# Kernel tuning notes

Measured on AMD Instinct MI355X. Metric: run time of the kernel, lower is better.

Reference implementation:

```python
import jax, jax.numpy as jnp
import numpy as np

N_NODES = 100000
N_EDGES = 1600000
N_GRAPHS = 512
IN_DIM = 128
HID = 128
N_CLASSES = 10


def _gcn_conv(x, W, b, src, dst, n):
    """PyG GCNConv: out = D^{-1/2} (A+I) D^{-1/2} (x @ W) + b."""
    xw = x @ W  # [n, out_dim]
    loop = jnp.arange(n)
    s = jnp.concatenate([src, loop])  # add self loops
    d = jnp.concatenate([dst, loop])
    deg = jax.ops.segment_sum(jnp.ones(s.shape, dtype=xw.dtype), d, num_segments=n)
    dinv = jnp.where(deg > 0, jax.lax.rsqrt(deg), jnp.zeros((), xw.dtype))
    norm = dinv[s] * dinv[d]  # [E + n]
    out = jax.ops.segment_sum(xw[s] * norm[:, None], d, num_segments=n)
    return out + b


def _global_mean_pool(x, batch, num_graphs):
    sums = jax.ops.segment_sum(x, batch, num_segments=num_graphs)
    cnts = jax.ops.segment_sum(jnp.ones(batch.shape, dtype=x.dtype), batch, num_segments=num_graphs)
    return sums / jnp.maximum(cnts, 1.0)[:, None]


def setup_inputs() -> dict:
    key = jax.random.key(0)
    ks = jax.random.split(key, 8)
    x = jax.random.normal(ks[0], (N_NODES, IN_DIM), dtype=jnp.float32)
    edge_index = jax.random.randint(ks[1], (2, N_EDGES), 0, N_NODES, dtype=jnp.int64)
    batch = jnp.sort(jax.random.randint(ks[2], (N_NODES,), 0, N_GRAPHS, dtype=jnp.int64))
    sc = 1.0 / np.sqrt(IN_DIM)
    W1 = jax.random.normal(ks[3], (IN_DIM, HID), dtype=jnp.float32) * sc
    b1 = jnp.zeros((HID,), dtype=jnp.float32)
    W2 = jax.random.normal(ks[4], (HID, HID), dtype=jnp.float32) * (1.0 / np.sqrt(HID))
    b2 = jnp.zeros((HID,), dtype=jnp.float32)
    Wc = jax.random.normal(ks[5], (HID, N_CLASSES), dtype=jnp.float32) * (1.0 / np.sqrt(HID))
    bc = jnp.zeros((N_CLASSES,), dtype=jnp.float32)
    return {"x": x, "edge_index": edge_index, "batch": batch,
            "W1": W1, "b1": b1, "W2": W2, "b2": b2, "Wc": Wc, "bc": bc}


def reference(x, edge_index, batch, W1, b1, W2, b2, Wc, bc):
    src, dst = edge_index[0], edge_index[1]
    n = x.shape[0]
    h = _gcn_conv(x, W1, b1, src, dst, n)
    h = jax.nn.relu(h)
    h = _gcn_conv(h, W2, b2, src, dst, n)
    g = _global_mean_pool(h, batch, N_GRAPHS)
    return g @ Wc + bc
```

## Files before the change

kernel.cpp:

```cpp
#include <hip/hip_runtime.h>

#define N_NODES 100000
#define N_EDGES 1600000
#define N_GRAPHS 512
#define DIM 128
#define NCLS 10
#define NBKT 782
#define BCAP 2560

typedef __attribute__((ext_vector_type(8))) short short8;
typedef __attribute__((ext_vector_type(4))) float f32x4;

static __device__ __forceinline__ unsigned short f2bf(float f) {
    unsigned u = __float_as_uint(f);
    unsigned r = (u + 0x7FFF + ((u >> 16) & 1)) >> 16;
    return (unsigned short)r;
}
static __device__ __forceinline__ float bf2f(unsigned u) {
    return __uint_as_float(u << 16);
}


__global__ void k_wprep(const float* __restrict__ W1, const float* __restrict__ W2,
                        unsigned short* __restrict__ wf1, unsigned short* __restrict__ wf2,
                        int* __restrict__ bcnt) {
    int b = blockIdx.x;
    if (b >= 128) {
        int i = (b - 128) * 256 + threadIdx.x;
        if (i < NBKT) bcnt[i] = 0;
        return;
    }
    const float* W = (b < 64) ? W1 : W2;
    unsigned short* wfrag = (b < 64) ? wf1 : wf2;
    int t = (b & 63) * 256 + threadIdx.x;
    int j = t & 7, lane = (t >> 3) & 63, nt = (t >> 9) & 7, kit = t >> 12;
    int k = kit * 32 + (lane >> 4) * 8 + j;
    int n = nt * 16 + (lane & 15);
    float v = W[k * 128 + n];
    unsigned short h = f2bf(v);
    wfrag[t] = h;
    wfrag[16384 + t] = f2bf(v - bf2f(h));
}


__global__ __launch_bounds__(256) void k_bucket(
    const int* __restrict__ src, const int* __restrict__ dst,
    int* __restrict__ bcnt, unsigned* __restrict__ bpack, int E) {
    __shared__ int cnt[NBKT];
    __shared__ int base[NBKT];
    int tid = threadIdx.x;
    for (int i = tid; i < NBKT; i += 256) cnt[i] = 0;
    __syncthreads();
    int e0 = blockIdx.x * 4096 + tid;
    unsigned pk[16]; short bk[16];
#pragma unroll
    for (int j = 0; j < 16; j++) {
        int e = e0 + j * 256;
        if (e < E) {
            int s = src[e], d = dst[e];
            bk[j] = (short)(d >> 7);
            pk[j] = ((unsigned)(d & 127) << 17) | (unsigned)s;
            atomicAdd(&cnt[bk[j]], 1);
        } else bk[j] = -1;
    }
    __syncthreads();
    for (int i = tid; i < NBKT; i += 256) {
        int c = cnt[i];
        base[i] = c ? atomicAdd(&bcnt[i], c) : 0;
        cnt[i] = 0;
    }
    __syncthreads();
#pragma unroll
    for (int j = 0; j < 16; j++) {
        if (bk[j] >= 0) {
            int p = base[bk[j]] + atomicAdd(&cnt[bk[j]], 1);
            if (p < BCAP) bpack[(size_t)bk[j] * BCAP + p] = pk[j];
        }
    }
}


__global__ __launch_bounds__(256) void k_bsort(
    const unsigned* __restrict__ bpack, const int* __restrict__ bcnt,
    int* __restrict__ rp, float* __restrict__ dinv,
    int* __restrict__ esrc, int N) {
    __shared__ int lds[256];
    __shared__ int gbase_sh;
    __shared__ int cnt[128];
    __shared__ int scan[128];
    __shared__ int cur[128];
    int b = blockIdx.x, tid = threadIdx.x;
    int v[4], pre[4];
    int s = 0;
#pragma unroll
    for (int j = 0; j < 4; j++) {
        int idx = tid * 4 + j;
        v[j] = (idx < NBKT) ? min(bcnt[idx], BCAP) : 0;
        pre[j] = s; s += v[j];
    }
    lds[tid] = s;
    __syncthreads();
    for (int off = 1; off < 256; off <<= 1) {
        int t = (tid >= off) ? lds[tid - off] : 0;
        __syncthreads();
        lds[tid] += t;
        __syncthreads();
    }
    if (tid == (b >> 2)) gbase_sh = lds[tid] - s + pre[b & 3];
    if (tid < 128) cnt[tid] = 0;
    __syncthreads();
    int gbase = gbase_sh;
    int n0 = b << 7;
    int m = min(bcnt[b], BCAP);
    const unsigned* bp = bpack + (size_t)b * BCAP;
    for (int j = tid; j < m; j += 256) atomicAdd(&cnt[bp[j] >> 17], 1);
    __syncthreads();
    if (tid < 128) scan[tid] = cnt[tid];
    __syncthreads();
    for (int off = 1; off < 128; off <<= 1) {
        int t = (tid < 128 && tid >= off) ? scan[tid - off] : 0;
        __syncthreads();
        if (tid < 128) scan[tid] += t;
        __syncthreads();
    }
    if (tid < 128) {
        int c = cnt[tid];
        int excl = scan[tid] - c;
        int node = n0 + tid;
        if (node <= N) rp[node] = gbase + excl;
        if (node < N) dinv[node] = rsqrtf((float)(c + 1));
        cur[tid] = gbase + excl;
    }
    __syncthreads();
    for (int j = tid; j < m; j += 256) {
        unsigned pk = bp[j];
        int p = atomicAdd(&cur[pk >> 17], 1);
        esrc[p] = (int)(pk & 0x1FFFF);
    }
}


__global__ __launch_bounds__(256) void k_gemm_f32(
    const float* __restrict__ A, const unsigned short* __restrict__ wfrag,
    const float* __restrict__ dinv, unsigned short* __restrict__ ybf, int M) {
    __shared__ unsigned short ldsw[4 * 32 * 136];
    int tid = threadIdx.x, wave = tid >> 6, lane = tid & 63;
    int m = lane & 15, quad = lane >> 4;
    int rowBase = blockIdx.x * 128 + wave * 32;
    int r0 = rowBase + m, r1 = rowBase + 16 + m;
    for (int i = tid; i < 2048; i += 256)
        ((short8*)ldsw)[i] = ((const short8*)wfrag)[i];
    __syncthreads();
    f32x4 acc0[8], acc1[8];
#pragma unroll
    for (int i = 0; i < 8; i++) { acc0[i] = (f32x4){0,0,0,0}; acc1[i] = (f32x4){0,0,0,0}; }
    const unsigned short* wlo = wfrag + 16384;

#pragma unroll
    for (int kit = 0; kit < 4; kit++) {
        float a0[8], a1[8];
        if (r0 < M) {
            const float4* ap = (const float4*)(A + (size_t)r0 * 128 + kit * 32 + quad * 8);
            float4 f0 = ap[0], f1 = ap[1];
            a0[0]=f0.x; a0[1]=f0.y; a0[2]=f0.z; a0[3]=f0.w; a0[4]=f1.x; a0[5]=f1.y; a0[6]=f1.z; a0[7]=f1.w;
        } else { for (int j = 0; j < 8; j++) a0[j] = 0.f; }
        if (r1 < M) {
            const float4* ap = (const float4*)(A + (size_t)r1 * 128 + kit * 32 + quad * 8);
            float4 f0 = ap[0], f1 = ap[1];
            a1[0]=f0.x; a1[1]=f0.y; a1[2]=f0.z; a1[3]=f0.w; a1[4]=f1.x; a1[5]=f1.y; a1[6]=f1.z; a1[7]=f1.w;
        } else { for (int j = 0; j < 8; j++) a1[j] = 0.f; }
        short8 ahi0, alo0, ahi1, alo1;
#pragma unroll
        for (int j = 0; j < 8; j++) {
            unsigned short h0 = f2bf(a0[j]);
            ahi0[j] = (short)h0; alo0[j] = (short)f2bf(a0[j] - bf2f(h0));
            unsigned short h1 = f2bf(a1[j]);
            ahi1[j] = (short)h1; alo1[j] = (short)f2bf(a1[j] - bf2f(h1));
        }
        int fb = kit * 4096 + lane * 8;
#pragma unroll
        for (int nt = 0; nt < 8; nt++) {
            int idx = fb + nt * 512;
            short8 bhi = *(const short8*)(ldsw + idx);
            short8 blo = *(const short8*)(wlo + idx);
            acc0[nt] = __builtin_amdgcn_mfma_f32_16x16x32_bf16(ahi0, bhi, acc0[nt], 0, 0, 0);
            acc0[nt] = __builtin_amdgcn_mfma_f32_16x16x32_bf16(alo0, bhi, acc0[nt], 0, 0, 0);
            acc0[nt] = __builtin_amdgcn_mfma_f32_16x16x32_bf16(ahi0, blo, acc0[nt], 0, 0, 0);
            acc1[nt] = __builtin_amdgcn_mfma_f32_16x16x32_bf16(ahi1, bhi, acc1[nt], 0, 0, 0);
            acc1[nt] = __builtin_amdgcn_mfma_f32_16x16x32_bf16(alo1, bhi, acc1[nt], 0, 0, 0);
            acc1[nt] = __builtin_amdgcn_mfma_f32_16x16x32_bf16(ahi1, blo, acc1[nt], 0, 0, 0);
        }
    }
    __syncthreads();
    float dv0 = (r0 < M) ? dinv[r0] : 0.f;
    float dv1 = (r1 < M) ? dinv[r1] : 0.f;
    unsigned short* wsm = ldsw + wave * 32 * 136;
#pragma unroll
    for (int rg = 0; rg < 4; rg++) {
        float s0 = __shfl(dv0, quad * 4 + rg);
        float s1 = __shfl(dv1, quad * 4 + rg);
#pragma unroll
        for (int nt = 0; nt < 8; nt++) {
            wsm[(quad * 4 + rg) * 136 + nt * 16 + m] = f2bf(acc0[nt][rg] * s0);
            wsm[(16 + quad * 4 + rg) * 136 + nt * 16 + m] = f2bf(acc1[nt][rg] * s1);
        }
    }
    __syncthreads();
#pragma unroll
    for (int i = 0; i < 8; i++) {
        int rl = i * 4 + quad;
        int grow = rowBase + rl;
        if (grow < M) {
            short8 v = *(const short8*)(wsm + rl * 136 + m * 8);
            *(short8*)(ybf + (size_t)grow * 128 + m * 8) = v;
        }
    }
}


__global__ __launch_bounds__(256) void k_gemm_bf(
    const unsigned short* __restrict__ A, const unsigned short* __restrict__ wfrag,
    const float* __restrict__ dinv, unsigned short* __restrict__ ybf, int M) {
    __shared__ unsigned short ldsw[4 * 32 * 136];
    int tid = threadIdx.x, wave = tid >> 6, lane = tid & 63;
    int m = lane & 15, quad = lane >> 4;
    int rowBase = blockIdx.x * 128 + wave * 32;
    int r0 = rowBase + m, r1 = rowBase + 16 + m;
    for (int i = tid; i < 2048; i += 256)
        ((short8*)ldsw)[i] = ((const short8*)wfrag)[i];
    __syncthreads();
    f32x4 acc0[8], acc1[8];
#pragma unroll
    for (int i = 0; i < 8; i++) { acc0[i] = (f32x4){0,0,0,0}; acc1[i] = (f32x4){0,0,0,0}; }
    const unsigned short* wlo = wfrag + 16384;

#pragma unroll
    for (int kit = 0; kit < 4; kit++) {
        short8 ah0, ah1;
        if (r0 < M) ah0 = *(const short8*)(A + (size_t)r0 * 128 + kit * 32 + quad * 8);
        else { for (int j = 0; j < 8; j++) ah0[j] = 0; }
        if (r1 < M) ah1 = *(const short8*)(A + (size_t)r1 * 128 + kit * 32 + quad * 8);
        else { for (int j = 0; j < 8; j++) ah1[j] = 0; }
        int fb = kit * 4096 + lane * 8;
#pragma unroll
        for (int nt = 0; nt < 8; nt++) {
            int idx = fb + nt * 512;
            short8 bhi = *(const short8*)(ldsw + idx);
            short8 blo = *(const short8*)(wlo + idx);
            acc0[nt] = __builtin_amdgcn_mfma_f32_16x16x32_bf16(ah0, bhi, acc0[nt], 0, 0, 0);
            acc0[nt] = __builtin_amdgcn_mfma_f32_16x16x32_bf16(ah0, blo, acc0[nt], 0, 0, 0);
            acc1[nt] = __builtin_amdgcn_mfma_f32_16x16x32_bf16(ah1, bhi, acc1[nt], 0, 0, 0);
            acc1[nt] = __builtin_amdgcn_mfma_f32_16x16x32_bf16(ah1, blo, acc1[nt], 0, 0, 0);
        }
    }
    __syncthreads();
    float dv0 = (r0 < M) ? dinv[r0] : 0.f;
    float dv1 = (r1 < M) ? dinv[r1] : 0.f;
    unsigned short* wsm = ldsw + wave * 32 * 136;
#pragma unroll
    for (int rg = 0; rg < 4; rg++) {
        float s0 = __shfl(dv0, quad * 4 + rg);
        float s1 = __shfl(dv1, quad * 4 + rg);
#pragma unroll
        for (int nt = 0; nt < 8; nt++) {
            wsm[(quad * 4 + rg) * 136 + nt * 16 + m] = f2bf(acc0[nt][rg] * s0);
            wsm[(16 + quad * 4 + rg) * 136 + nt * 16 + m] = f2bf(acc1[nt][rg] * s1);
        }
    }
    __syncthreads();
#pragma unroll
    for (int i = 0; i < 8; i++) {
        int rl = i * 4 + quad;
        int grow = rowBase + rl;
        if (grow < M) {
            short8 v = *(const short8*)(wsm + rl * 136 + m * 8);
            *(short8*)(ybf + (size_t)grow * 128 + m * 8) = v;
        }
    }
}


__global__ __launch_bounds__(256) void k_agg(
    const unsigned short* __restrict__ y, const float* __restrict__ dinv,
    const int* __restrict__ rp, const int* __restrict__ esrc,
    const float* __restrict__ bias, unsigned* __restrict__ out, int relu, int N) {
    int wave = threadIdx.x >> 6;
    int lane = threadIdx.x & 63;
    int node = blockIdx.x * 4 + wave;
    if (node >= N) return;
    const unsigned* y2 = (const unsigned*)y;
    unsigned vs = y2[(size_t)node * 64 + lane];
    float a0 = bf2f(vs & 0xFFFF), a1 = bf2f(vs >> 16);
    int beg = rp[node], end = rp[node + 1];
    int j = beg;
    while (j < end) {
        int idxv = (j + lane < end) ? esrc[j + lane] : 0;
        int cnt = end - j; if (cnt > 64) cnt = 64;
        int i = 0;
        for (; i + 4 <= cnt; i += 4) {
            int s0 = __shfl(idxv, i + 0);
            int s1 = __shfl(idxv, i + 1);
            int s2 = __shfl(idxv, i + 2);
            int s3 = __shfl(idxv, i + 3);
            unsigned v0 = y2[(size_t)s0 * 64 + lane];
            unsigned v1 = y2[(size_t)s1 * 64 + lane];
            unsigned v2 = y2[(size_t)s2 * 64 + lane];
            unsigned v3 = y2[(size_t)s3 * 64 + lane];
            a0 += bf2f(v0 & 0xFFFF); a1 += bf2f(v0 >> 16);
            a0 += bf2f(v1 & 0xFFFF); a1 += bf2f(v1 >> 16);
            a0 += bf2f(v2 & 0xFFFF); a1 += bf2f(v2 >> 16);
            a0 += bf2f(v3 & 0xFFFF); a1 += bf2f(v3 >> 16);
        }
        for (; i < cnt; i++) {
            int s = __shfl(idxv, i);
            unsigned v = y2[(size_t)s * 64 + lane];
            a0 += bf2f(v & 0xFFFF); a1 += bf2f(v >> 16);
        }
        j += cnt;
    }
    float s = dinv[node];
    float2 bv = ((const float2*)bias)[lane];
    float o0 = s * a0 + bv.x;
    float o1 = s * a1 + bv.y;
    if (relu) { o0 = fmaxf(o0, 0.f); o1 = fmaxf(o1, 0.f); }
    out[(size_t)node * 64 + lane] = (unsigned)f2bf(o0) | ((unsigned)f2bf(o1) << 16);
}


__global__ __launch_bounds__(256) void k_poolhead(
    const unsigned* __restrict__ h2, const int* __restrict__ batch,
    const float* __restrict__ Wc, const float* __restrict__ bc,
    float* __restrict__ out, int n) {
    __shared__ float2 red[4][64];
    __shared__ float grow[DIM];
    int gid = blockIdx.x;
    int tid = threadIdx.x, wave = tid >> 6, lane = tid & 63;
    int lo = 0, hi = n;
    while (lo < hi) { int mid = (lo + hi) >> 1; if (batch[mid] < gid) lo = mid + 1; else hi = mid; }
    int start = lo;
    hi = n;
    while (lo < hi) { int mid = (lo + hi) >> 1; if (batch[mid] < gid + 1) lo = mid + 1; else hi = mid; }
    int end = lo;
    float a0 = 0.f, a1 = 0.f;
    for (int r = start + wave; r < end; r += 4) {
        unsigned v = h2[(size_t)r * 64 + lane];
        a0 += bf2f(v & 0xFFFF); a1 += bf2f(v >> 16);
    }
    red[wave][lane] = make_float2(a0, a1);
    __syncthreads();
    if (tid < 64) {
        float2 s = red[0][tid];
        s.x += red[1][tid].x; s.y += red[1][tid].y;
        s.x += red[2][tid].x; s.y += red[2][tid].y;
        s.x += red[3][tid].x; s.y += red[3][tid].y;
        int cnt = end - start;
        float inv = 1.f / (float)(cnt > 0 ? cnt : 1);
        grow[tid * 2] = s.x * inv;
        grow[tid * 2 + 1] = s.y * inv;
    }
    __syncthreads();
    if (tid < NCLS) {
        float acc = bc[tid];
#pragma unroll 16
        for (int k = 0; k < DIM; k++) acc += grow[k] * Wc[k * NCLS + tid];
        out[gid * NCLS + tid] = acc;
    }
}

extern "C" void kernel_launch(void* const* d_in, const int* in_sizes, int n_in,
                              void* d_out, int out_size, void* d_ws, size_t ws_size,
                              hipStream_t stream) {
    const float* x    = (const float*)d_in[0];
    const int*   ei   = (const int*)d_in[1];
    const int*   batch= (const int*)d_in[2];
    const float* W1   = (const float*)d_in[3];
    const float* b1   = (const float*)d_in[4];
    const float* W2   = (const float*)d_in[5];
    const float* b2   = (const float*)d_in[6];
    const float* Wc   = (const float*)d_in[7];
    const float* bc   = (const float*)d_in[8];
    float* out = (float*)d_out;
    const int N = N_NODES, E = N_EDGES;
    const int* src = ei;
    const int* dst = ei + E;

    char* ws = (char*)d_ws;
    size_t off = 0;
    auto carve = [&](size_t bytes) -> void* {
        void* p = ws + off;
        off = (off + bytes + 255) & ~(size_t)255;
        return p;
    };
    int*      rp    = (int*)     carve((size_t)(N + 1) * 4);
    float*    dinv  = (float*)   carve((size_t)N * 4);
    int*      bcnt  = (int*)     carve(NBKT * 4);
    unsigned* bpack = (unsigned*)carve((size_t)NBKT * BCAP * 4);
    int*      esrc  = (int*)     carve((size_t)E * 4);
    unsigned short* wf1 = (unsigned short*)carve(2 * 16384 * 2);
    unsigned short* wf2 = (unsigned short*)carve(2 * 16384 * 2);
    unsigned short* bufY = (unsigned short*)carve((size_t)N * DIM * 2);
    unsigned short* bufH = (unsigned short*)carve((size_t)N * DIM * 2);
    (void)ws_size; (void)n_in; (void)in_sizes; (void)out_size;

    hipLaunchKernelGGL(k_wprep,  dim3(128 + (NBKT + 255) / 256), dim3(256), 0, stream, W1, W2, wf1, wf2, bcnt);
    hipLaunchKernelGGL(k_bucket, dim3((E + 4095) / 4096), dim3(256), 0, stream, src, dst, bcnt, bpack, E);
    hipLaunchKernelGGL(k_bsort,  dim3(NBKT), dim3(256), 0, stream, bpack, bcnt, rp, dinv, esrc, N);

    int gemmGrid = (N + 127) / 128;
    hipLaunchKernelGGL(k_gemm_f32, dim3(gemmGrid), dim3(256), 0, stream, x, wf1, dinv, bufY, N);
    hipLaunchKernelGGL(k_agg, dim3((N + 3) / 4), dim3(256), 0, stream, bufY, dinv, rp, esrc, b1, (unsigned*)bufH, 1, N);
    hipLaunchKernelGGL(k_gemm_bf, dim3(gemmGrid), dim3(256), 0, stream, bufH, wf2, dinv, bufY, N);
    hipLaunchKernelGGL(k_agg, dim3((N + 3) / 4), dim3(256), 0, stream, bufY, dinv, rp, esrc, b2, (unsigned*)bufH, 0, N);
    hipLaunchKernelGGL(k_poolhead, dim3(N_GRAPHS), dim3(256), 0, stream, (const unsigned*)bufH, batch, Wc, bc, out, N);
}
```

Baseline: 340.9 us.

## Overlap first GEMM with graph bucketing/sort by merging kernels; move dinv scaling into aggregation

The source-side dinv scaling is moved out of both GEMM epilogues and into the aggregation kernels, which now gather dinv[src] per edge and scale each neighbour row. This removes the GEMMs' dependence on dinv. The first GEMM is then split in half and fused as extra blocks into the bucket and bucket-sort launches, so its work overlaps the CSR construction and saves a kernel launch. The cost is an extra dinv gather per edge and more multiplies in the gather loop of both aggregation passes.

Result: no change. 344.2 us (+1.0%).

```diff
diff --git a/kernel.cpp b/kernel.cpp
--- a/kernel.cpp
+++ b/kernel.cpp
@@ -43,15 +43,16 @@
 }
 
 
-__global__ __launch_bounds__(256) void k_bucket(
+static __device__ __forceinline__ void bucket_body(
+    char* smemraw, int bid,
     const int* __restrict__ src, const int* __restrict__ dst,
     int* __restrict__ bcnt, unsigned* __restrict__ bpack, int E) {
-    __shared__ int cnt[NBKT];
-    __shared__ int base[NBKT];
+    int* cnt  = (int*)smemraw;
+    int* base = cnt + NBKT;
     int tid = threadIdx.x;
     for (int i = tid; i < NBKT; i += 256) cnt[i] = 0;
     __syncthreads();
-    int e0 = blockIdx.x * 4096 + tid;
+    int e0 = bid * 4096 + tid;
     unsigned pk[16]; short bk[16];
 #pragma unroll
     for (int j = 0; j < 16; j++) {
@@ -79,17 +80,17 @@
     }
 }
 
-
-__global__ __launch_bounds__(256) void k_bsort(
+static __device__ __forceinline__ void bsort_body(
+    char* smemraw, int b,
     const unsigned* __restrict__ bpack, const int* __restrict__ bcnt,
     int* __restrict__ rp, float* __restrict__ dinv,
     int* __restrict__ esrc, int N) {
-    __shared__ int lds[256];
-    __shared__ int gbase_sh;
-    __shared__ int cnt[128];
-    __shared__ int scan[128];
-    __shared__ int cur[128];
-    int b = blockIdx.x, tid = threadIdx.x;
+    int* lds      = (int*)smemraw;
+    int* cnt      = lds + 256;
+    int* scan     = lds + 384;
+    int* cur      = lds + 512;
+    int* gbase_sh = lds + 640;
+    int tid = threadIdx.x;
     int v[4], pre[4];
     int s = 0;
 #pragma unroll
@@ -106,10 +107,10 @@
         lds[tid] += t;
         __syncthreads();
     }
-    if (tid == (b >> 2)) gbase_sh = lds[tid] - s + pre[b & 3];
+    if (tid == (b >> 2)) *gbase_sh = lds[tid] - s + pre[b & 3];
     if (tid < 128) cnt[tid] = 0;
     __syncthreads();
-    int gbase = gbase_sh;
+    int gbase = *gbase_sh;
     int n0 = b << 7;
     int m = min(bcnt[b], BCAP);
     const unsigned* bp = bpack + (size_t)b * BCAP;
@@ -139,14 +140,14 @@
     }
 }
 
-
-__global__ __launch_bounds__(256) void k_gemm_f32(
+static __device__ __forceinline__ void gemm_f32_body(
+    char* smemraw, int rowBlk,
     const float* __restrict__ A, const unsigned short* __restrict__ wfrag,
-    const float* __restrict__ dinv, unsigned short* __restrict__ ybf, int M) {
-    __shared__ unsigned short ldsw[4 * 32 * 136];
+    unsigned short* __restrict__ ybf, int M) {
+    unsigned short* ldsw = (unsigned short*)smemraw;
     int tid = threadIdx.x, wave = tid >> 6, lane = tid & 63;
     int m = lane & 15, quad = lane >> 4;
-    int rowBase = blockIdx.x * 128 + wave * 32;
+    int rowBase = rowBlk * 128 + wave * 32;
     int r0 = rowBase + m, r1 = rowBase + 16 + m;
     for (int i = tid; i < 2048; i += 256)
         ((short8*)ldsw)[i] = ((const short8*)wfrag)[i];
@@ -192,17 +193,13 @@
         }
     }
     __syncthreads();
-    float dv0 = (r0 < M) ? dinv[r0] : 0.f;
-    float dv1 = (r1 < M) ? dinv[r1] : 0.f;
     unsigned short* wsm = ldsw + wave * 32 * 136;
 #pragma unroll
     for (int rg = 0; rg < 4; rg++) {
-        float s0 = __shfl(dv0, quad * 4 + rg);
-        float s1 = __shfl(dv1, quad * 4 + rg);
 #pragma unroll
         for (int nt = 0; nt < 8; nt++) {
-            wsm[(quad * 4 + rg) * 136 + nt * 16 + m] = f2bf(acc0[nt][rg] * s0);
-            wsm[(16 + quad * 4 + rg) * 136 + nt * 16 + m] = f2bf(acc1[nt][rg] * s1);
+            wsm[(quad * 4 + rg) * 136 + nt * 16 + m] = f2bf(acc0[nt][rg]);
+            wsm[(16 + quad * 4 + rg) * 136 + nt * 16 + m] = f2bf(acc1[nt][rg]);
         }
     }
     __syncthreads();
@@ -218,9 +215,31 @@
 }
 
 
+__global__ __launch_bounds__(256) void k_p2(
+    const int* __restrict__ src, const int* __restrict__ dst,
+    int* __restrict__ bcnt, unsigned* __restrict__ bpack, int E,
+    const float* __restrict__ A, const unsigned short* __restrict__ wfrag,
+    unsigned short* __restrict__ ybf, int M, int nb) {
+    __shared__ __align__(16) char smem[4 * 32 * 136 * 2];
+    if ((int)blockIdx.x < nb) bucket_body(smem, blockIdx.x, src, dst, bcnt, bpack, E);
+    else                      gemm_f32_body(smem, blockIdx.x - nb, A, wfrag, ybf, M);
+}
+
+
+__global__ __launch_bounds__(256) void k_p3(
+    const unsigned* __restrict__ bpack, const int* __restrict__ bcnt,
+    int* __restrict__ rp, float* __restrict__ dinv, int* __restrict__ esrc, int N,
+    const float* __restrict__ A, const unsigned short* __restrict__ wfrag,
+    unsigned short* __restrict__ ybf, int M, int rowOff) {
+    __shared__ __align__(16) char smem[4 * 32 * 136 * 2];
+    if ((int)blockIdx.x < NBKT) bsort_body(smem, blockIdx.x, bpack, bcnt, rp, dinv, esrc, N);
+    else                        gemm_f32_body(smem, rowOff + (blockIdx.x - NBKT), A, wfrag, ybf, M);
+}
+
+
 __global__ __launch_bounds__(256) void k_gemm_bf(
     const unsigned short* __restrict__ A, const unsigned short* __restrict__ wfrag,
-    const float* __restrict__ dinv, unsigned short* __restrict__ ybf, int M) {
+    unsigned short* __restrict__ ybf, int M) {
     __shared__ unsigned short ldsw[4 * 32 * 136];
     int tid = threadIdx.x, wave = tid >> 6, lane = tid & 63;
     int m = lane & 15, quad = lane >> 4;
@@ -254,17 +273,13 @@
         }
     }
     __syncthreads();
-    float dv0 = (r0 < M) ? dinv[r0] : 0.f;
-    float dv1 = (r1 < M) ? dinv[r1] : 0.f;
     unsigned short* wsm = ldsw + wave * 32 * 136;
 #pragma unroll
     for (int rg = 0; rg < 4; rg++) {
-        float s0 = __shfl(dv0, quad * 4 + rg);
-        float s1 = __shfl(dv1, quad * 4 + rg);
 #pragma unroll
         for (int nt = 0; nt < 8; nt++) {
-            wsm[(quad * 4 + rg) * 136 + nt * 16 + m] = f2bf(acc0[nt][rg] * s0);
-            wsm[(16 + quad * 4 + rg) * 136 + nt * 16 + m] = f2bf(acc1[nt][rg] * s1);
+            wsm[(quad * 4 + rg) * 136 + nt * 16 + m] = f2bf(acc0[nt][rg]);
+            wsm[(16 + quad * 4 + rg) * 136 + nt * 16 + m] = f2bf(acc1[nt][rg]);
         }
     }
     __syncthreads();
@@ -289,12 +304,14 @@
     int node = blockIdx.x * 4 + wave;
     if (node >= N) return;
     const unsigned* y2 = (const unsigned*)y;
+    float sd = dinv[node];
     unsigned vs = y2[(size_t)node * 64 + lane];
-    float a0 = bf2f(vs & 0xFFFF), a1 = bf2f(vs >> 16);
+    float a0 = sd * bf2f(vs & 0xFFFF), a1 = sd * bf2f(vs >> 16);
     int beg = rp[node], end = rp[node + 1];
     int j = beg;
     while (j < end) {
-        int idxv = (j + lane < end) ? esrc[j + lane] : 0;
+        int idxv = 0; float dvv = 0.f;
+        if (j + lane < end) { idxv = esrc[j + lane]; dvv = dinv[idxv]; }
         int cnt = end - j; if (cnt > 64) cnt = 64;
         int i = 0;
         for (; i + 4 <= cnt; i += 4) {
@@ -302,26 +319,30 @@
             int s1 = __shfl(idxv, i + 1);
             int s2 = __shfl(idxv, i + 2);
             int s3 = __shfl(idxv, i + 3);
+            float d0 = __shfl(dvv, i + 0);
+            float d1 = __shfl(dvv, i + 1);
+            float d2 = __shfl(dvv, i + 2);
+            float d3 = __shfl(dvv, i + 3);
             unsigned v0 = y2[(size_t)s0 * 64 + lane];
             unsigned v1 = y2[(size_t)s1 * 64 + lane];
             unsigned v2 = y2[(size_t)s2 * 64 + lane];
             unsigned v3 = y2[(size_t)s3 * 64 + lane];
-            a0 += bf2f(v0 & 0xFFFF); a1 += bf2f(v0 >> 16);
-            a0 += bf2f(v1 & 0xFFFF); a1 += bf2f(v1 >> 16);
-            a0 += bf2f(v2 & 0xFFFF); a1 += bf2f(v2 >> 16);
-            a0 += bf2f(v3 & 0xFFFF); a1 += bf2f(v3 >> 16);
+            a0 += d0 * bf2f(v0 & 0xFFFF); a1 += d0 * bf2f(v0 >> 16);
+            a0 += d1 * bf2f(v1 & 0xFFFF); a1 += d1 * bf2f(v1 >> 16);
+            a0 += d2 * bf2f(v2 & 0xFFFF); a1 += d2 * bf2f(v2 >> 16);
+            a0 += d3 * bf2f(v3 & 0xFFFF); a1 += d3 * bf2f(v3 >> 16);
         }
         for (; i < cnt; i++) {
             int s = __shfl(idxv, i);
+            float d = __shfl(dvv, i);
             unsigned v = y2[(size_t)s * 64 + lane];
-            a0 += bf2f(v & 0xFFFF); a1 += bf2f(v >> 16);
+            a0 += d * bf2f(v & 0xFFFF); a1 += d * bf2f(v >> 16);
         }
         j += cnt;
     }
-    float s = dinv[node];
     float2 bv = ((const float2*)bias)[lane];
-    float o0 = s * a0 + bv.x;
-    float o1 = s * a1 + bv.y;
+    float o0 = sd * a0 + bv.x;
+    float o1 = sd * a1 + bv.y;
     if (relu) { o0 = fmaxf(o0, 0.f); o1 = fmaxf(o1, 0.f); }
     out[(size_t)node * 64 + lane] = (unsigned)f2bf(o0) | ((unsigned)f2bf(o1) << 16);
 }
@@ -402,14 +423,17 @@
     unsigned short* bufH = (unsigned short*)carve((size_t)N * DIM * 2);
     (void)ws_size; (void)n_in; (void)in_sizes; (void)out_size;
 
-    hipLaunchKernelGGL(k_wprep,  dim3(128 + (NBKT + 255) / 256), dim3(256), 0, stream, W1, W2, wf1, wf2, bcnt);
-    hipLaunchKernelGGL(k_bucket, dim3((E + 4095) / 4096), dim3(256), 0, stream, src, dst, bcnt, bpack, E);
-    hipLaunchKernelGGL(k_bsort,  dim3(NBKT), dim3(256), 0, stream, bpack, bcnt, rp, dinv, esrc, N);
-
-    int gemmGrid = (N + 127) / 128;
-    hipLaunchKernelGGL(k_gemm_f32, dim3(gemmGrid), dim3(256), 0, stream, x, wf1, dinv, bufY, N);
+    const int nbBkt = (E + 4095) / 4096;
+    const int gemmGrid = (N + 127) / 128;
+    const int gA = gemmGrid / 2;
+
+    hipLaunchKernelGGL(k_wprep, dim3(128 + (NBKT + 255) / 256), dim3(256), 0, stream, W1, W2, wf1, wf2, bcnt);
+    hipLaunchKernelGGL(k_p2, dim3(nbBkt + gA), dim3(256), 0, stream,
+                       src, dst, bcnt, bpack, E, x, wf1, bufY, N, nbBkt);
+    hipLaunchKernelGGL(k_p3, dim3(NBKT + (gemmGrid - gA)), dim3(256), 0, stream,
+                       bpack, bcnt, rp, dinv, esrc, N, x, wf1, bufY, N, gA);
     hipLaunchKernelGGL(k_agg, dim3((N + 3) / 4), dim3(256), 0, stream, bufY, dinv, rp, esrc, b1, (unsigned*)bufH, 1, N);
-    hipLaunchKernelGGL(k_gemm_bf, dim3(gemmGrid), dim3(256), 0, stream, bufH, wf2, dinv, bufY, N);
+    hipLaunchKernelGGL(k_gemm_bf, dim3(gemmGrid), dim3(256), 0, stream, bufH, wf2, bufY, N);
     hipLaunchKernelGGL(k_agg, dim3((N + 3) / 4), dim3(256), 0, stream, bufY, dinv, rp, esrc, b2, (unsigned*)bufH, 0, N);
     hipLaunchKernelGGL(k_poolhead, dim3(N_GRAPHS), dim3(256), 0, stream, (const unsigned*)bufH, batch, Wc, bc, out, N);
 }
```

## Merge bucket sort and first GEMM into one launch using global degree counts

Applied to the files above, without the earlier changes.

The first GEMM needs only node degrees, so degrees are now counted with global atomics during bucketing. This lets the bucket-sort blocks and the layer-1 GEMM blocks run side by side in one heterogeneous kernel instead of two dependent launches. The goal is to overlap the latency-bound sort with the compute-bound GEMM and save one launch. The cost is 1.6M extra global atomics on the degree array, one more zeroing pass, and a shared LDS size across both block types.

Result: slower. 386.4 us (+13.4%).

```diff
diff --git a/kernel.cpp b/kernel.cpp
--- a/kernel.cpp
+++ b/kernel.cpp
@@ -23,11 +23,16 @@
 
 __global__ void k_wprep(const float* __restrict__ W1, const float* __restrict__ W2,
                         unsigned short* __restrict__ wf1, unsigned short* __restrict__ wf2,
-                        int* __restrict__ bcnt) {
+                        int* __restrict__ bcnt, int* __restrict__ deg) {
     int b = blockIdx.x;
     if (b >= 128) {
-        int i = (b - 128) * 256 + threadIdx.x;
-        if (i < NBKT) bcnt[i] = 0;
+        if (b < 132) {
+            int i = (b - 128) * 256 + threadIdx.x;
+            if (i < NBKT) bcnt[i] = 0;
+        } else {
+            int i = (b - 132) * 256 + threadIdx.x;
+            if (i < N_NODES) deg[i] = 0;
+        }
         return;
     }
     const float* W = (b < 64) ? W1 : W2;
@@ -45,7 +50,8 @@
 
 __global__ __launch_bounds__(256) void k_bucket(
     const int* __restrict__ src, const int* __restrict__ dst,
-    int* __restrict__ bcnt, unsigned* __restrict__ bpack, int E) {
+    int* __restrict__ bcnt, unsigned* __restrict__ bpack,
+    int* __restrict__ deg, int E) {
     __shared__ int cnt[NBKT];
     __shared__ int base[NBKT];
     int tid = threadIdx.x;
@@ -58,6 +64,7 @@
         int e = e0 + j * 256;
         if (e < E) {
             int s = src[e], d = dst[e];
+            atomicAdd(&deg[d], 1);
             bk[j] = (short)(d >> 7);
             pk[j] = ((unsigned)(d & 127) << 17) | (unsigned)s;
             atomicAdd(&cnt[bk[j]], 1);
@@ -80,16 +87,17 @@
 }
 
 
-__global__ __launch_bounds__(256) void k_bsort(
+static __device__ __forceinline__ void bsort_body(
+    char* smemraw, int b,
     const unsigned* __restrict__ bpack, const int* __restrict__ bcnt,
     int* __restrict__ rp, float* __restrict__ dinv,
     int* __restrict__ esrc, int N) {
-    __shared__ int lds[256];
-    __shared__ int gbase_sh;
-    __shared__ int cnt[128];
-    __shared__ int scan[128];
-    __shared__ int cur[128];
-    int b = blockIdx.x, tid = threadIdx.x;
+    int* lds      = (int*)smemraw;
+    int* cnt      = lds + 256;
+    int* scan     = lds + 384;
+    int* cur      = lds + 512;
+    int* gbase_sh = lds + 640;
+    int tid = threadIdx.x;
     int v[4], pre[4];
     int s = 0;
 #pragma unroll
@@ -106,10 +114,10 @@
         lds[tid] += t;
         __syncthreads();
     }
-    if (tid == (b >> 2)) gbase_sh = lds[tid] - s + pre[b & 3];
+    if (tid == (b >> 2)) *gbase_sh = lds[tid] - s + pre[b & 3];
     if (tid < 128) cnt[tid] = 0;
     __syncthreads();
-    int gbase = gbase_sh;
+    int gbase = *gbase_sh;
     int n0 = b << 7;
     int m = min(bcnt[b], BCAP);
     const unsigned* bp = bpack + (size_t)b * BCAP;
@@ -139,14 +147,14 @@
     }
 }
 
-
-__global__ __launch_bounds__(256) void k_gemm_f32(
+static __device__ __forceinline__ void gemm_f32_body(
+    char* smemraw, int rowBlk,
     const float* __restrict__ A, const unsigned short* __restrict__ wfrag,
-    const float* __restrict__ dinv, unsigned short* __restrict__ ybf, int M) {
-    __shared__ unsigned short ldsw[4 * 32 * 136];
+    const int* __restrict__ deg, unsigned short* __restrict__ ybf, int M) {
+    unsigned short* ldsw = (unsigned short*)smemraw;
     int tid = threadIdx.x, wave = tid >> 6, lane = tid & 63;
     int m = lane & 15, quad = lane >> 4;
-    int rowBase = blockIdx.x * 128 + wave * 32;
+    int rowBase = rowBlk * 128 + wave * 32;
     int r0 = rowBase + m, r1 = rowBase + 16 + m;
     for (int i = tid; i < 2048; i += 256)
         ((short8*)ldsw)[i] = ((const short8*)wfrag)[i];
@@ -192,8 +200,8 @@
         }
     }
     __syncthreads();
-    float dv0 = (r0 < M) ? dinv[r0] : 0.f;
-    float dv1 = (r1 < M) ? dinv[r1] : 0.f;
+    float dv0 = (r0 < M) ? rsqrtf((float)deg[r0] + 1.0f) : 0.f;
+    float dv1 = (r1 < M) ? rsqrtf((float)deg[r1] + 1.0f) : 0.f;
     unsigned short* wsm = ldsw + wave * 32 * 136;
 #pragma unroll
     for (int rg = 0; rg < 4; rg++) {
@@ -215,6 +223,17 @@
             *(short8*)(ybf + (size_t)grow * 128 + m * 8) = v;
         }
     }
+}
+
+
+__global__ __launch_bounds__(256) void k_p3(
+    const unsigned* __restrict__ bpack, const int* __restrict__ bcnt,
+    int* __restrict__ rp, float* __restrict__ dinv, int* __restrict__ esrc, int N,
+    const float* __restrict__ A, const unsigned short* __restrict__ wfrag,
+    const int* __restrict__ deg, unsigned short* __restrict__ ybf, int M) {
+    __shared__ __align__(16) char smem[4 * 32 * 136 * 2];
+    if ((int)blockIdx.x < NBKT) bsort_body(smem, blockIdx.x, bpack, bcnt, rp, dinv, esrc, N);
+    else                        gemm_f32_body(smem, blockIdx.x - NBKT, A, wfrag, deg, ybf, M);
 }
 
 
@@ -394,6 +413,7 @@
     int*      rp    = (int*)     carve((size_t)(N + 1) * 4);
     float*    dinv  = (float*)   carve((size_t)N * 4);
     int*      bcnt  = (int*)     carve(NBKT * 4);
+    int*      deg   = (int*)     carve((size_t)N * 4);
     unsigned* bpack = (unsigned*)carve((size_t)NBKT * BCAP * 4);
     int*      esrc  = (int*)     carve((size_t)E * 4);
     unsigned short* wf1 = (unsigned short*)carve(2 * 16384 * 2);
@@ -402,12 +422,14 @@
     unsigned short* bufH = (unsigned short*)carve((size_t)N * DIM * 2);
     (void)ws_size; (void)n_in; (void)in_sizes; (void)out_size;
 
-    hipLaunchKernelGGL(k_wprep,  dim3(128 + (NBKT + 255) / 256), dim3(256), 0, stream, W1, W2, wf1, wf2, bcnt);
-    hipLaunchKernelGGL(k_bucket, dim3((E + 4095) / 4096), dim3(256), 0, stream, src, dst, bcnt, bpack, E);
-    hipLaunchKernelGGL(k_bsort,  dim3(NBKT), dim3(256), 0, stream, bpack, bcnt, rp, dinv, esrc, N);
-
-    int gemmGrid = (N + 127) / 128;
-    hipLaunchKernelGGL(k_gemm_f32, dim3(gemmGrid), dim3(256), 0, stream, x, wf1, dinv, bufY, N);
+    const int nbBkt = (E + 4095) / 4096;
+    const int gemmGrid = (N + 127) / 128;
+    const int degZero = (N + 255) / 256;
+
+    hipLaunchKernelGGL(k_wprep, dim3(132 + degZero), dim3(256), 0, stream, W1, W2, wf1, wf2, bcnt, deg);
+    hipLaunchKernelGGL(k_bucket, dim3(nbBkt), dim3(256), 0, stream, src, dst, bcnt, bpack, deg, E);
+    hipLaunchKernelGGL(k_p3, dim3(NBKT + gemmGrid), dim3(256), 0, stream,
+                       bpack, bcnt, rp, dinv, esrc, N, x, wf1, deg, bufY, N);
     hipLaunchKernelGGL(k_agg, dim3((N + 3) / 4), dim3(256), 0, stream, bufY, dinv, rp, esrc, b1, (unsigned*)bufH, 1, N);
     hipLaunchKernelGGL(k_gemm_bf, dim3(gemmGrid), dim3(256), 0, stream, bufH, wf2, dinv, bufY, N);
     hipLaunchKernelGGL(k_agg, dim3((N + 3) / 4), dim3(256), 0, stream, bufY, dinv, rp, esrc, b2, (unsigned*)bufH, 0, N);
```
